# Kernel optimization log

Measured on AMD Instinct MI355X. Metric: run time of the kernel, lower is better.

Reference implementation:

```python
import jax, jax.numpy as jnp
import numpy as np

B, H, W, C = 32, 64, 64, 256


def setup_inputs() -> dict:
    key = jax.random.key(0)
    ks = jax.random.split(key, 4)
    scale = 1.0 / np.sqrt(C)
    return {
        "x": jax.random.normal(ks[0], (B, H, W, C), dtype=jnp.float32),
        "wq": jax.random.normal(ks[1], (C, C), dtype=jnp.float32) * scale,
        "bq": jnp.zeros((C,), dtype=jnp.float32),
        "wk": jax.random.normal(ks[2], (C, C), dtype=jnp.float32) * scale,
        "bk": jnp.zeros((C,), dtype=jnp.float32),
        "wv": jax.random.normal(ks[3], (C, C), dtype=jnp.float32) * scale,
        "bv": jnp.zeros((C,), dtype=jnp.float32),
    }


def reference(x, wq, bq, wk, bk, wv, bv):
    # 1x1 convs == per-pixel dense projections
    q = jnp.einsum('bhwc,cf->bhwf', x, wq) + bq
    k = jnp.einsum('bhwc,cf->bhwf', x, wk) + bk
    v = jnp.einsum('bhwc,cf->bhwf', x, wv) + bv
    # tf.matmul(key, query, transpose_b=True): batch dims (b,h), contract over c
    attn = jnp.einsum('bhwc,bhvc->bhwv', k, q)  # [B,H,W,W], NO 1/sqrt(d) scaling
    attn = jax.nn.softmax(attn, axis=-1)
    out = jnp.einsum('bhwv,bhvc->bhwc', attn, v)  # [B,H,W,C]
    return out * x  # elementwise gate with raw input
```

## Files before the change

### kernel.cpp

```cpp
#include <hip/hip_runtime.h>

#define CD   256
#define WD   64
#define NBH  2048
#define XST  264
#define VST  72
#define SST  68

typedef unsigned short u16;
typedef __attribute__((ext_vector_type(8))) short bfrag_t;
typedef __attribute__((ext_vector_type(4))) float f4_t;

#define MFMA(a, b, c) __builtin_amdgcn_mfma_f32_16x16x32_bf16(a, b, c, 0, 0, 0)

__device__ __forceinline__ u16 f2bf(float f) {
    unsigned u = __float_as_uint(f);
    u += 0x7fffu + ((u >> 16) & 1u);
    return (u16)(u >> 16);
}
__device__ __forceinline__ float bf2f(u16 h) {
    return __uint_as_float(((unsigned)h) << 16);
}

__global__ __launch_bounds__(256) void prep_m(
    const float* __restrict__ wq, const float* __restrict__ wk,
    u16* __restrict__ Mthi, u16* __restrict__ Mtlo)
{
    __shared__ float swq[16 * 257];
    __shared__ float swk[32 * 257];
    const int t = threadIdx.x;
    const int dt = blockIdx.x >> 3;
    const int ct = blockIdx.x & 7;
    #pragma unroll
    for (int n = 0; n < 16; ++n) {
        int idx = n * 256 + t;
        int d = idx >> 8, f = idx & 255;
        swq[d * 257 + f] = wq[(dt * 16 + d) * CD + f];
    }
    #pragma unroll
    for (int n = 0; n < 32; ++n) {
        int idx = n * 256 + t;
        int c = idx >> 8, f = idx & 255;
        swk[c * 257 + f] = wk[(ct * 32 + c) * CD + f];
    }
    __syncthreads();
    const int d = t & 15, c0 = (t >> 4) * 2;
    #pragma unroll
    for (int cc = 0; cc < 2; ++cc) {
        const float* kr = &swk[(c0 + cc) * 257];
        const float* qr = &swq[d * 257];
        float acc = 0.f;
        #pragma unroll 8
        for (int f = 0; f < CD; ++f) acc = fmaf(kr[f], qr[f], acc);
        u16 h = f2bf(acc);
        int off = (dt * 16 + d) * CD + ct * 32 + c0 + cc;
        Mthi[off] = h;
        Mtlo[off] = f2bf(acc - bf2f(h));
    }
}

__global__ __launch_bounds__(256) void prep_v(
    const float* __restrict__ wv, u16* __restrict__ Wvthi)
{
    __shared__ float tile[64 * 65];
    const int t = threadIdx.x;
    const int bc = blockIdx.x >> 2, bd = blockIdx.x & 3;
    #pragma unroll
    for (int n = 0; n < 16; ++n) {
        int idx = n * 256 + t;
        int c = idx >> 6, d = idx & 63;
        tile[c * 65 + d] = wv[(bc * 64 + c) * CD + bd * 64 + d];
    }
    __syncthreads();
    #pragma unroll
    for (int n = 0; n < 16; ++n) {
        int idx = n * 256 + t;
        int d = idx >> 6, c = idx & 63;
        Wvthi[(bd * 64 + d) * CD + bc * 64 + c] = f2bf(tile[c * 65 + d]);
    }
}

__global__ __launch_bounds__(256) void prep_b(
    const float* __restrict__ wq, const float* __restrict__ bk,
    float* __restrict__ wqbk)
{
    __shared__ float sbk[CD];
    const int t = threadIdx.x;
    if (t < CD) sbk[t] = bk[t];
    __syncthreads();
    const int c = blockIdx.x * 16 + (t >> 4), part = t & 15;
    const float* wr = wq + c * CD + part * 16;
    const float* br = sbk + part * 16;
    float a = 0.f;
    #pragma unroll
    for (int j = 0; j < 16; ++j) a = fmaf(wr[j], br[j], a);
    a += __shfl_xor(a, 1);
    a += __shfl_xor(a, 2);
    a += __shfl_xor(a, 4);
    a += __shfl_xor(a, 8);
    if (part == 0) wqbk[c] = a;
}

extern __shared__ char smem_raw[];

__global__ __launch_bounds__(1024, 4) void attn_kernel(
    const float* __restrict__ x,
    const u16* __restrict__ Mthi, const u16* __restrict__ Mtlo,
    const u16* __restrict__ Wvthi, const float* __restrict__ wqbk,
    const float* __restrict__ bv, float* __restrict__ out)
{
    u16* sXhi = (u16*)smem_raw;
    u16* sXlo = sXhi + WD * XST;
    u16* sThi = sXlo + WD * XST;
    u16* sTlo = sThi + WD * XST;
    u16* sVt  = sThi;
    float* sS  = (float*)(sTlo + WD * XST);
    float* sxb = sS + WD * SST;
    float* sbv = sxb + WD;

    const int t = threadIdx.x;
    const int wave = t >> 6, lane = t & 63;
    const int lane15 = lane & 15, quad = lane >> 4;
    const int bh = blockIdx.x;
    const float* __restrict__ xblk = x + (size_t)bh * (WD * CD);
    float* __restrict__ oblk = out + (size_t)bh * (WD * CD);

    if (t < CD) sbv[t] = bv[t];
    {
        const float4* xv4 = (const float4*)xblk;
        #pragma unroll
        for (int n = 0; n < 4; ++n) {
            int idx = n * 1024 + t;
            float4 v = xv4[idx];
            int i = idx >> 6;
            int c = (idx & 63) << 2;
            ushort4 h4, l4;
            h4.x = f2bf(v.x); l4.x = f2bf(v.x - bf2f(h4.x));
            h4.y = f2bf(v.y); l4.y = f2bf(v.y - bf2f(h4.y));
            h4.z = f2bf(v.z); l4.z = f2bf(v.z - bf2f(h4.z));
            h4.w = f2bf(v.w); l4.w = f2bf(v.w - bf2f(h4.w));
            *(ushort4*)&sXhi[i * XST + c] = h4;
            *(ushort4*)&sXlo[i * XST + c] = l4;
        }
    }
    {
        const int row = t >> 4, part = t & 15;
        const float* xr = xblk + row * CD + part * 16;
        const float* br = wqbk + part * 16;
        float a = 0.f;
        #pragma unroll
        for (int i = 0; i < 4; ++i) {
            float4 xv = *(const float4*)&xr[i * 4];
            float4 bvv = *(const float4*)&br[i * 4];
            a = fmaf(xv.x, bvv.x, a); a = fmaf(xv.y, bvv.y, a);
            a = fmaf(xv.z, bvv.z, a); a = fmaf(xv.w, bvv.w, a);
        }
        a += __shfl_xor(a, 1);
        a += __shfl_xor(a, 2);
        a += __shfl_xor(a, 4);
        a += __shfl_xor(a, 8);
        if (part == 0) sxb[row] = a;
    }
    __syncthreads();

    f4_t accV[4];
    {
        f4_t accT[4];
        const f4_t z = {0.f, 0.f, 0.f, 0.f};
        #pragma unroll
        for (int a = 0; a < 4; ++a) { accT[a] = z; accV[a] = z; }

        const int drow = wave * 16 + lane15;
        #pragma unroll
        for (int kk = 0; kk < 8; ++kk) {
            const int k0 = kk * 32 + quad * 8;
            const int mo = drow * CD + k0;
            bfrag_t Ah = *(const bfrag_t*)(Mthi + mo);
            bfrag_t Al = *(const bfrag_t*)(Mtlo + mo);
            bfrag_t Av = *(const bfrag_t*)(Wvthi + mo);
            bfrag_t Bh[4], Bl[4];
            #pragma unroll
            for (int nt = 0; nt < 4; ++nt) {
                const int xo = (nt * 16 + lane15) * XST + k0;
                Bh[nt] = *(const bfrag_t*)(sXhi + xo);
                Bl[nt] = *(const bfrag_t*)(sXlo + xo);
            }
            #pragma unroll
            for (int nt = 0; nt < 4; ++nt) {
                accT[nt] = MFMA(Ah, Bh[nt], accT[nt]);
                accT[nt] = MFMA(Ah, Bl[nt], accT[nt]);
                accT[nt] = MFMA(Al, Bh[nt], accT[nt]);
                accV[nt] = MFMA(Av, Bh[nt], accV[nt]);
            }
        }
        #pragma unroll
        for (int nt = 0; nt < 4; ++nt) {
            const int i  = nt * 16 + lane15;
            const int d0 = wave * 16 + quad * 4;
            ushort4 h4, l4;
            float f;
            f = accT[nt][0]; h4.x = f2bf(f); l4.x = f2bf(f - bf2f(h4.x));
            f = accT[nt][1]; h4.y = f2bf(f); l4.y = f2bf(f - bf2f(h4.y));
            f = accT[nt][2]; h4.z = f2bf(f); l4.z = f2bf(f - bf2f(h4.z));
            f = accT[nt][3]; h4.w = f2bf(f); l4.w = f2bf(f - bf2f(h4.w));
            *(ushort4*)&sThi[i * XST + d0] = h4;
            *(ushort4*)&sTlo[i * XST + d0] = l4;
        }
    }
    __syncthreads();

    {
        f4_t acc = {0.f, 0.f, 0.f, 0.f};
        const int m0 = (wave >> 2) * 16;
        const int n0 = (wave & 3) * 16;
        #pragma unroll
        for (int kk = 0; kk < 8; ++kk) {
            const int k0 = kk * 32 + quad * 8;
            const int to = (m0 + lane15) * XST + k0;
            const int xo = (n0 + lane15) * XST + k0;
            bfrag_t Th = *(const bfrag_t*)(sThi + to);
            bfrag_t Tl = *(const bfrag_t*)(sTlo + to);
            bfrag_t Xh = *(const bfrag_t*)(sXhi + xo);
            bfrag_t Xl = *(const bfrag_t*)(sXlo + xo);
            acc = MFMA(Th, Xh, acc);
            acc = MFMA(Th, Xl, acc);
            acc = MFMA(Tl, Xh, acc);
        }
        const int v = n0 + lane15;
        const float xbv = sxb[v];
        #pragma unroll
        for (int r = 0; r < 4; ++r) {
            const int wtok = m0 + quad * 4 + r;
            sS[wtok * SST + v] = acc[r] + xbv;
        }
    }
    __syncthreads();

    {
        const int drow0 = wave * 16 + quad * 4;
        #pragma unroll
        for (int nt = 0; nt < 4; ++nt) {
            const int j = nt * 16 + lane15;
            #pragma unroll
            for (int r = 0; r < 4; ++r) {
                const int d = drow0 + r;
                sVt[d * VST + j] = f2bf(accV[nt][r] + sbv[d]);
            }
        }
    }
    {
        const int row = t >> 4, part = t & 15;
        float* srow = &sS[row * SST + part * 4];
        float e[4];
        float mx = fmaxf(fmaxf(srow[0], srow[1]), fmaxf(srow[2], srow[3]));
        mx = fmaxf(mx, __shfl_xor(mx, 1));
        mx = fmaxf(mx, __shfl_xor(mx, 2));
        mx = fmaxf(mx, __shfl_xor(mx, 4));
        mx = fmaxf(mx, __shfl_xor(mx, 8));
        float sum = 0.f;
        #pragma unroll
        for (int u = 0; u < 4; ++u) { e[u] = __expf(srow[u] - mx); sum += e[u]; }
        sum += __shfl_xor(sum, 1);
        sum += __shfl_xor(sum, 2);
        sum += __shfl_xor(sum, 4);
        sum += __shfl_xor(sum, 8);
        float inv = 1.0f / sum;
        #pragma unroll
        for (int u = 0; u < 4; ++u) srow[u] = e[u] * inv;
    }
    __syncthreads();

    {
        f4_t acc[4];
        const f4_t z = {0.f, 0.f, 0.f, 0.f};
        #pragma unroll
        for (int a = 0; a < 4; ++a) acc[a] = z;

        const int m0 = (wave & 3) * 16;
        const int nbase = (wave >> 2) * 64;
        #pragma unroll
        for (int kk = 0; kk < 2; ++kk) {
            const int k0 = kk * 32 + quad * 8;
            const float* p = &sS[(m0 + lane15) * SST + k0];
            f4_t p0 = *(const f4_t*)p;
            f4_t p1 = *(const f4_t*)(p + 4);
            bfrag_t Af;
            Af[0] = (short)f2bf(p0[0]); Af[1] = (short)f2bf(p0[1]);
            Af[2] = (short)f2bf(p0[2]); Af[3] = (short)f2bf(p0[3]);
            Af[4] = (short)f2bf(p1[0]); Af[5] = (short)f2bf(p1[1]);
            Af[6] = (short)f2bf(p1[2]); Af[7] = (short)f2bf(p1[3]);
            #pragma unroll
            for (int nt = 0; nt < 4; ++nt) {
                bfrag_t Bf = *(const bfrag_t*)(sVt + (nbase + nt * 16 + lane15) * VST + k0);
                acc[nt] = MFMA(Af, Bf, acc[nt]);
            }
        }
        #pragma unroll
        for (int nt = 0; nt < 4; ++nt) {
            const int d = nbase + nt * 16 + lane15;
            #pragma unroll
            for (int r = 0; r < 4; ++r) {
                const int wtok = m0 + quad * 4 + r;
                float g = xblk[wtok * CD + d];
                oblk[wtok * CD + d] = acc[nt][r] * g;
            }
        }
    }
}

extern "C" void kernel_launch(void* const* d_in, const int* in_sizes, int n_in,
                              void* d_out, int out_size, void* d_ws, size_t ws_size,
                              hipStream_t stream) {
    const float* x  = (const float*)d_in[0];
    const float* wq = (const float*)d_in[1];
    const float* wk = (const float*)d_in[3];
    const float* bk = (const float*)d_in[4];
    const float* wv = (const float*)d_in[5];
    const float* bv = (const float*)d_in[6];
    float* out = (float*)d_out;

    char* ws = (char*)d_ws;
    u16* Mthi   = (u16*)ws;
    u16* Mtlo   = (u16*)(ws + (128 << 10));
    u16* Wvthi  = (u16*)(ws + (256 << 10));
    float* wqbk = (float*)(ws + (384 << 10));

    prep_m<<<128, 256, 0, stream>>>(wq, wk, Mthi, Mtlo);
    prep_v<<<16, 256, 0, stream>>>(wv, Wvthi);
    prep_b<<<16, 256, 0, stream>>>(wq, bk, wqbk);

    const size_t lds = (size_t)(4 * WD * XST * sizeof(u16)) +
                       (WD * SST + WD + CD) * sizeof(float);
    hipFuncSetAttribute((const void*)attn_kernel,
                        hipFuncAttributeMaxDynamicSharedMemorySize, (int)lds);
    attn_kernel<<<NBH, 1024, lds, stream>>>(x, Mthi, Mtlo, Wvthi, wqbk, bv, out);
}
```

Baseline: 416.5 us.

## Switch projection and PV GEMMs to 32x32x16 MFMA tiles per wave

```diff
diff --git a/kernel.cpp b/kernel.cpp
--- a/kernel.cpp
+++ b/kernel.cpp
@@ -10,8 +10,10 @@
 typedef unsigned short u16;
 typedef __attribute__((ext_vector_type(8))) short bfrag_t;
 typedef __attribute__((ext_vector_type(4))) float f4_t;
-
-#define MFMA(a, b, c) __builtin_amdgcn_mfma_f32_16x16x32_bf16(a, b, c, 0, 0, 0)
+typedef __attribute__((ext_vector_type(16))) float f16f_t;
+
+#define MFMA16(a, b, c) __builtin_amdgcn_mfma_f32_16x16x32_bf16(a, b, c, 0, 0, 0)
+#define MFMA32(a, b, c) __builtin_amdgcn_mfma_f32_32x32x16_bf16(a, b, c, 0, 0, 0)
 
 __device__ __forceinline__ u16 f2bf(float f) {
     unsigned u = __float_as_uint(f);
@@ -121,6 +123,7 @@
     const int t = threadIdx.x;
     const int wave = t >> 6, lane = t & 63;
     const int lane15 = lane & 15, quad = lane >> 4;
+    const int lane31 = lane & 31, kh = lane >> 5;
     const int bh = blockIdx.x;
     const float* __restrict__ xblk = x + (size_t)bh * (WD * CD);
     float* __restrict__ oblk = out + (size_t)bh * (WD * CD);
@@ -163,48 +166,38 @@
     }
     __syncthreads();
 
-    f4_t accV[4];
-    {
-        f4_t accT[4];
-        const f4_t z = {0.f, 0.f, 0.f, 0.f};
-        #pragma unroll
-        for (int a = 0; a < 4; ++a) { accT[a] = z; accV[a] = z; }
-
-        const int drow = wave * 16 + lane15;
-        #pragma unroll
-        for (int kk = 0; kk < 8; ++kk) {
-            const int k0 = kk * 32 + quad * 8;
-            const int mo = drow * CD + k0;
-            bfrag_t Ah = *(const bfrag_t*)(Mthi + mo);
-            bfrag_t Al = *(const bfrag_t*)(Mtlo + mo);
-            bfrag_t Av = *(const bfrag_t*)(Wvthi + mo);
-            bfrag_t Bh[4], Bl[4];
-            #pragma unroll
-            for (int nt = 0; nt < 4; ++nt) {
-                const int xo = (nt * 16 + lane15) * XST + k0;
-                Bh[nt] = *(const bfrag_t*)(sXhi + xo);
-                Bl[nt] = *(const bfrag_t*)(sXlo + xo);
-            }
-            #pragma unroll
-            for (int nt = 0; nt < 4; ++nt) {
-                accT[nt] = MFMA(Ah, Bh[nt], accT[nt]);
-                accT[nt] = MFMA(Ah, Bl[nt], accT[nt]);
-                accT[nt] = MFMA(Al, Bh[nt], accT[nt]);
-                accV[nt] = MFMA(Av, Bh[nt], accV[nt]);
-            }
-        }
-        #pragma unroll
-        for (int nt = 0; nt < 4; ++nt) {
-            const int i  = nt * 16 + lane15;
-            const int d0 = wave * 16 + quad * 4;
+    {
+        const int dt32 = wave >> 1;
+        const int tt32 = wave & 1;
+        f16f_t acc;
+        #pragma unroll
+        for (int i = 0; i < 16; ++i) acc[i] = 0.f;
+
+        const int arow = dt32 * 32 + lane31;
+        const int brow = tt32 * 32 + lane31;
+        #pragma unroll
+        for (int kk = 0; kk < 16; ++kk) {
+            const int k0 = kk * 16 + kh * 8;
+            bfrag_t Ah = *(const bfrag_t*)(Mthi + arow * CD + k0);
+            bfrag_t Al = *(const bfrag_t*)(Mtlo + arow * CD + k0);
+            bfrag_t Bh = *(const bfrag_t*)(sXhi + brow * XST + k0);
+            bfrag_t Bl = *(const bfrag_t*)(sXlo + brow * XST + k0);
+            acc = MFMA32(Ah, Bh, acc);
+            acc = MFMA32(Ah, Bl, acc);
+            acc = MFMA32(Al, Bh, acc);
+        }
+        const int tok = tt32 * 32 + lane31;
+        #pragma unroll
+        for (int rq = 0; rq < 4; ++rq) {
+            const int dbase = dt32 * 32 + rq * 8 + kh * 4;
             ushort4 h4, l4;
             float f;
-            f = accT[nt][0]; h4.x = f2bf(f); l4.x = f2bf(f - bf2f(h4.x));
-            f = accT[nt][1]; h4.y = f2bf(f); l4.y = f2bf(f - bf2f(h4.y));
-            f = accT[nt][2]; h4.z = f2bf(f); l4.z = f2bf(f - bf2f(h4.z));
-            f = accT[nt][3]; h4.w = f2bf(f); l4.w = f2bf(f - bf2f(h4.w));
-            *(ushort4*)&sThi[i * XST + d0] = h4;
-            *(ushort4*)&sTlo[i * XST + d0] = l4;
+            f = acc[rq * 4 + 0]; h4.x = f2bf(f); l4.x = f2bf(f - bf2f(h4.x));
+            f = acc[rq * 4 + 1]; h4.y = f2bf(f); l4.y = f2bf(f - bf2f(h4.y));
+            f = acc[rq * 4 + 2]; h4.z = f2bf(f); l4.z = f2bf(f - bf2f(h4.z));
+            f = acc[rq * 4 + 3]; h4.w = f2bf(f); l4.w = f2bf(f - bf2f(h4.w));
+            *(ushort4*)&sThi[tok * XST + dbase] = h4;
+            *(ushort4*)&sTlo[tok * XST + dbase] = l4;
         }
     }
     __syncthreads();
@@ -222,9 +215,9 @@
             bfrag_t Tl = *(const bfrag_t*)(sTlo + to);
             bfrag_t Xh = *(const bfrag_t*)(sXhi + xo);
             bfrag_t Xl = *(const bfrag_t*)(sXlo + xo);
-            acc = MFMA(Th, Xh, acc);
-            acc = MFMA(Th, Xl, acc);
-            acc = MFMA(Tl, Xh, acc);
+            acc = MFMA16(Th, Xh, acc);
+            acc = MFMA16(Th, Xl, acc);
+            acc = MFMA16(Tl, Xh, acc);
         }
         const int v = n0 + lane15;
         const float xbv = sxb[v];
@@ -237,14 +230,28 @@
     __syncthreads();
 
     {
-        const int drow0 = wave * 16 + quad * 4;
-        #pragma unroll
-        for (int nt = 0; nt < 4; ++nt) {
-            const int j = nt * 16 + lane15;
+        const int dt32 = wave >> 1;
+        const int tt32 = wave & 1;
+        f16f_t acc;
+        #pragma unroll
+        for (int i = 0; i < 16; ++i) acc[i] = 0.f;
+
+        const int arow = dt32 * 32 + lane31;
+        const int brow = tt32 * 32 + lane31;
+        #pragma unroll
+        for (int kk = 0; kk < 16; ++kk) {
+            const int k0 = kk * 16 + kh * 8;
+            bfrag_t Av = *(const bfrag_t*)(Wvthi + arow * CD + k0);
+            bfrag_t Bh = *(const bfrag_t*)(sXhi + brow * XST + k0);
+            acc = MFMA32(Av, Bh, acc);
+        }
+        const int j = tt32 * 32 + lane31;
+        #pragma unroll
+        for (int rq = 0; rq < 4; ++rq) {
             #pragma unroll
-            for (int r = 0; r < 4; ++r) {
-                const int d = drow0 + r;
-                sVt[d * VST + j] = f2bf(accV[nt][r] + sbv[d]);
+            for (int jj = 0; jj < 4; ++jj) {
+                const int d = dt32 * 32 + rq * 8 + kh * 4 + jj;
+                sVt[d * VST + j] = f2bf(acc[rq * 4 + jj] + sbv[d]);
             }
         }
     }
@@ -271,17 +278,18 @@
     __syncthreads();
 
     {
-        f4_t acc[4];
-        const f4_t z = {0.f, 0.f, 0.f, 0.f};
-        #pragma unroll
-        for (int a = 0; a < 4; ++a) acc[a] = z;
-
-        const int m0 = (wave & 3) * 16;
-        const int nbase = (wave >> 2) * 64;
-        #pragma unroll
-        for (int kk = 0; kk < 2; ++kk) {
-            const int k0 = kk * 32 + quad * 8;
-            const float* p = &sS[(m0 + lane15) * SST + k0];
+        const int wt32 = wave & 1;
+        const int dt32 = wave >> 1;
+        f16f_t acc;
+        #pragma unroll
+        for (int i = 0; i < 16; ++i) acc[i] = 0.f;
+
+        const int arow = wt32 * 32 + lane31;
+        const int brow = dt32 * 32 + lane31;
+        #pragma unroll
+        for (int kk = 0; kk < 4; ++kk) {
+            const int k0 = kk * 16 + kh * 8;
+            const float* p = &sS[arow * SST + k0];
             f4_t p0 = *(const f4_t*)p;
             f4_t p1 = *(const f4_t*)(p + 4);
             bfrag_t Af;
@@ -289,20 +297,17 @@
             Af[2] = (short)f2bf(p0[2]); Af[3] = (short)f2bf(p0[3]);
             Af[4] = (short)f2bf(p1[0]); Af[5] = (short)f2bf(p1[1]);
             Af[6] = (short)f2bf(p1[2]); Af[7] = (short)f2bf(p1[3]);
+            bfrag_t Bf = *(const bfrag_t*)(sVt + brow * VST + k0);
+            acc = MFMA32(Af, Bf, acc);
+        }
+        const int dcol = dt32 * 32 + lane31;
+        #pragma unroll
+        for (int rq = 0; rq < 4; ++rq) {
             #pragma unroll
-            for (int nt = 0; nt < 4; ++nt) {
-                bfrag_t Bf = *(const bfrag_t*)(sVt + (nbase + nt * 16 + lane15) * VST + k0);
-                acc[nt] = MFMA(Af, Bf, acc[nt]);
-            }
-        }
-        #pragma unroll
-        for (int nt = 0; nt < 4; ++nt) {
-            const int d = nbase + nt * 16 + lane15;
-            #pragma unroll
-            for (int r = 0; r < 4; ++r) {
-                const int wtok = m0 + quad * 4 + r;
-                float g = xblk[wtok * CD + d];
-                oblk[wtok * CD + d] = acc[nt][r] * g;
+            for (int jj = 0; jj < 4; ++jj) {
+                const int wtok = wt32 * 32 + rq * 8 + kh * 4 + jj;
+                float g = xblk[wtok * CD + dcol];
+                oblk[wtok * CD + dcol] = acc[rq * 4 + jj] * g;
             }
         }
     }
```

Result: slower. 458.5 us (+10.1%).
